# Kernel tuning notes

Hardware: AMD Instinct MI355X
Metric: run time of the kernel (lower is better)

Reference implementation:

```python
import jax, jax.numpy as jnp
import numpy as np

D_MODEL = 1024
N_HEADS = 16
HEAD = D_MODEL // N_HEADS  # 64
B, S = 4, 2048


def setup_inputs() -> dict:
    key = jax.random.key(0)
    ks = jax.random.split(key, 8)
    sd = 1.0 / np.sqrt(D_MODEL)
    return {
        "query": jax.random.normal(ks[0], (B, S, D_MODEL), jnp.float32),
        "key_in": jax.random.normal(ks[1], (B, S, D_MODEL), jnp.float32),
        "value": jax.random.normal(ks[2], (B, S, D_MODEL), jnp.float32),
        # per-head projections stacked: [H, d_model, head_size]
        "Wq": jax.random.normal(ks[3], (N_HEADS, D_MODEL, HEAD), jnp.float32) * sd,
        "Wk": jax.random.normal(ks[4], (N_HEADS, D_MODEL, HEAD), jnp.float32) * sd,
        "Wv": jax.random.normal(ks[5], (N_HEADS, D_MODEL, HEAD), jnp.float32) * sd,
        "Wo": jax.random.normal(ks[6], (D_MODEL, D_MODEL), jnp.float32) * sd,
        "bo": jax.random.normal(ks[7], (D_MODEL,), jnp.float32) * 0.01,
    }


def reference(query, key_in, value, Wq, Wk, Wv, Wo, bo):
    # batched per-head projections: [B,H,S,K]
    q = jnp.einsum("bsd,hdk->bhsk", query, Wq)
    k = jnp.einsum("bsd,hdk->bhsk", key_in, Wk)
    v = jnp.einsum("bsd,hdk->bhsk", value, Wv)
    # NOTE: original scales by sqrt(d_model) (query.shape[-1]), not sqrt(head_size)
    scale = 1.0 / np.sqrt(D_MODEL)
    scores = jnp.einsum("bhsk,bhtk->bhst", q, k) * scale  # [B,H,S,S]
    attn = jax.nn.softmax(scores, axis=-1)
    ctx = jnp.einsum("bhst,bhtk->bhsk", attn, v)  # [B,H,S,K]
    # concat heads -> [B,S,H*K]
    ctx = jnp.transpose(ctx, (0, 2, 1, 3)).reshape(B, S, D_MODEL)
    return ctx @ Wo.T + bo  # output linear (dropout = identity at eval)
```

## Files before the change

kernel.cpp:

```cpp
#include <hip/hip_runtime.h>
#include <stdint.h>

#define DM   1024
#define HD   64
#define SEQ  2048
#define NB   4
#define MR   8192

typedef __bf16  bf16x8 __attribute__((ext_vector_type(8)));
typedef float   f32x4  __attribute__((ext_vector_type(4)));
typedef unsigned short u16x8 __attribute__((ext_vector_type(8)));

__device__ __forceinline__ unsigned short f2bf(float f) {
  union { float f; unsigned u; } x; x.f = f;
  unsigned u = x.u + 0x7fffu + ((x.u >> 16) & 1u);
  return (unsigned short)(u >> 16);
}

__device__ __forceinline__ unsigned pk_bf16(float a, float b) {
  unsigned ua = __builtin_bit_cast(unsigned, a) + 0x8000u;
  unsigned ub = __builtin_bit_cast(unsigned, b) + 0x8000u;
  return __builtin_amdgcn_perm(ub, ua, 0x07060302);
}

__device__ __forceinline__ float fexp2(float x) {
#if __has_builtin(__builtin_amdgcn_exp2f)
  return __builtin_amdgcn_exp2f(x);
#else
  float r; asm("v_exp_f32 %0, %1" : "=v"(r) : "v"(x)); return r;
#endif
}

__device__ __forceinline__ void gld_lds16(const void* g, void* l) {
  __builtin_amdgcn_global_load_lds((const __attribute__((address_space(1))) unsigned int*)g,
                                   (__attribute__((address_space(3))) unsigned int*)l, 16, 0, 0);
}

__global__ __launch_bounds__(256) void cvt3(const float* __restrict__ a, const float* __restrict__ b,
                                            const float* __restrict__ c, unsigned short* __restrict__ oa,
                                            unsigned short* __restrict__ ob, unsigned short* __restrict__ oc) {
  const float* in = (blockIdx.z == 0) ? a : (blockIdx.z == 1) ? b : c;
  unsigned short* out = (blockIdx.z == 0) ? oa : (blockIdx.z == 1) ? ob : oc;
  size_t i = ((size_t)blockIdx.x * 256 + threadIdx.x) * 8;
  float4 x = *(const float4*)(in + i);
  float4 y = *(const float4*)(in + i + 4);
  u16x8 r = { f2bf(x.x), f2bf(x.y), f2bf(x.z), f2bf(x.w), f2bf(y.x), f2bf(y.y), f2bf(y.z), f2bf(y.w) };
  *(u16x8*)(out + i) = r;
}

__global__ __launch_bounds__(256) void wtrans(const float* __restrict__ wq, const float* __restrict__ wk,
                                              const float* __restrict__ wv, unsigned short* __restrict__ wt) {
  __shared__ float tile[64 * 65];
  const float* in = (blockIdx.z == 0) ? wq : (blockIdx.z == 1) ? wk : wv;
  unsigned short* out = wt + ((size_t)blockIdx.z << 20);
  const int h = blockIdx.x >> 4, d0 = (blockIdx.x & 15) * 64;
  const int tid = threadIdx.x;
  const int k = tid & 63, rr = tid >> 6;
#pragma unroll
  for (int j = 0; j < 16; ++j) {
    int row = rr + j * 4;
    tile[row * 65 + k] = in[h * 65536 + (d0 + row) * 64 + k];
  }
  __syncthreads();
  const int dd = tid & 63, kr = tid >> 6;
#pragma unroll
  for (int j = 0; j < 16; ++j) {
    int kk = kr + j * 4;
    out[(size_t)(h * 64 + kk) * 1024 + d0 + dd] = f2bf(tile[dd * 65 + kk]);
  }
}

__global__ __launch_bounds__(256) void cvt1(const float* __restrict__ in, unsigned short* __restrict__ out) {
  size_t i = ((size_t)blockIdx.x * 256 + threadIdx.x) * 8;
  float4 x = *(const float4*)(in + i);
  float4 y = *(const float4*)(in + i + 4);
  u16x8 r = { f2bf(x.x), f2bf(x.y), f2bf(x.z), f2bf(x.w), f2bf(y.x), f2bf(y.y), f2bf(y.z), f2bf(y.w) };
  *(u16x8*)(out + i) = r;
}

template <bool BF16OUT>
__global__ __launch_bounds__(256, 2) void gemm_bt(
    const unsigned short* __restrict__ A0, const unsigned short* __restrict__ A1,
    const unsigned short* __restrict__ A2, const unsigned short* __restrict__ Bt,
    void* __restrict__ Cv, const float* __restrict__ bias) {
  __shared__ char lds[32768];
  char* ldsA = lds;
  char* ldsB = lds + 16384;

  const int tid = threadIdx.x, w = tid >> 6, l = tid & 63;
  const int quad = l >> 4, l15 = l & 15;
  const int z = blockIdx.z;
  const unsigned short* A = (z == 0) ? A0 : (z == 1) ? A1 : A2;
  const unsigned short* B = Bt + (size_t)z * (DM * DM);
  const int lin = blockIdx.y * 8 + blockIdx.x;
  const int swz = (lin & 7) * 64 + (lin >> 3);
  const int bm = (swz >> 3) * 128, bn = (swz & 7) * 128;
  const int wrow = (w >> 1) * 64, wcol = (w & 1) * 64;

  const int srow = w * 32 + (l >> 3);
  const int sc   = ((l & 7) ^ ((l >> 3) & 7)) * 8;
  char* ldsAw = ldsA + (w * 32) * 128;
  char* ldsBw = ldsB + (w * 32) * 128;

  f32x4 acc[4][4];
#pragma unroll
  for (int i = 0; i < 4; ++i)
#pragma unroll
    for (int j = 0; j < 4; ++j) acc[i][j] = (f32x4){0.f, 0.f, 0.f, 0.f};

  for (int kt = 0; kt < DM; kt += 64) {
#pragma unroll
    for (int p = 0; p < 4; ++p) {
      gld_lds16(A + (size_t)(bm + srow + p * 8) * DM + kt + sc, ldsAw + p * 1024);
      gld_lds16(B + (size_t)(bn + srow + p * 8) * DM + kt + sc, ldsBw + p * 1024);
    }
    __syncthreads();
#pragma unroll
    for (int ks = 0; ks < 2; ++ks) {
      bf16x8 af[4], bfr[4];
#pragma unroll
      for (int mt = 0; mt < 4; ++mt) {
        int r = wrow + mt * 16 + l15;
        af[mt] = *(const bf16x8*)(ldsA + r * 128 + (((ks * 4 + quad) ^ (r & 7)) * 16));
      }
#pragma unroll
      for (int nt = 0; nt < 4; ++nt) {
        int r = wcol + nt * 16 + l15;
        bfr[nt] = *(const bf16x8*)(ldsB + r * 128 + (((ks * 4 + quad) ^ (r & 7)) * 16));
      }
#pragma unroll
      for (int mt = 0; mt < 4; ++mt)
#pragma unroll
        for (int nt = 0; nt < 4; ++nt)
          acc[mt][nt] = __builtin_amdgcn_mfma_f32_16x16x32_bf16(af[mt], bfr[nt], acc[mt][nt], 0, 0, 0);
    }
    __syncthreads();
  }

  if constexpr (BF16OUT) {
    unsigned short* C = (unsigned short*)Cv + (size_t)z * ((size_t)MR * DM);
#pragma unroll
    for (int mt = 0; mt < 4; ++mt)
#pragma unroll
      for (int r = 0; r < 4; ++r) {
        size_t row = bm + wrow + mt * 16 + quad * 4 + r;
#pragma unroll
        for (int nt = 0; nt < 4; ++nt)
          C[row * DM + bn + wcol + nt * 16 + l15] = f2bf(acc[mt][nt][r]);
      }
  } else {
    float* C = (float*)Cv;
    float bv[4];
#pragma unroll
    for (int nt = 0; nt < 4; ++nt) bv[nt] = bias[bn + wcol + nt * 16 + l15];
#pragma unroll
    for (int mt = 0; mt < 4; ++mt)
#pragma unroll
      for (int r = 0; r < 4; ++r) {
        size_t row = bm + wrow + mt * 16 + quad * 4 + r;
#pragma unroll
        for (int nt = 0; nt < 4; ++nt)
          C[row * DM + bn + wcol + nt * 16 + l15] = acc[mt][nt][r] + bv[nt];
      }
  }
}

__global__ __launch_bounds__(512, 4) void attn_flash(
    const unsigned short* __restrict__ Qp, const unsigned short* __restrict__ Kp,
    const unsigned short* __restrict__ Vp, unsigned short* __restrict__ Ctx) {
  __shared__ char lds[65536];
  char* ldsK  = lds;
  char* ldsVt = lds + 16384;
  char* ldsP  = lds + 32768;

  const int tid = threadIdx.x, w = tid >> 6, l = tid & 63;
  const int quad = l >> 4, l15 = l & 15;
  const int lin = blockIdx.y * 8 + blockIdx.x;
  const int swz = (lin & 7) * 64 + (lin >> 3);
  const int qt = swz & 7, bh = swz >> 3;
  const int b = bh >> 4, h = bh & 15;
  const size_t rb = (size_t)b * SEQ;
  const int hc = h * HD;

  bf16x8 qf[2][2];
  const int q0 = qt * 256 + w * 32;
#pragma unroll
  for (int mt = 0; mt < 2; ++mt)
#pragma unroll
    for (int ks = 0; ks < 2; ++ks)
      qf[mt][ks] = *(const bf16x8*)(Qp + (rb + q0 + mt * 16 + l15) * DM + hc + ks * 32 + quad * 8);

  f32x4 o[2][4], l_acc[2];
#pragma unroll
  for (int mt = 0; mt < 2; ++mt) {
    l_acc[mt] = (f32x4){0.f, 0.f, 0.f, 0.f};
#pragma unroll
    for (int nt = 0; nt < 4; ++nt) o[mt][nt] = (f32x4){0.f, 0.f, 0.f, 0.f};
  }

  const int sc = ((l & 7) ^ (l >> 3)) * 8;
  const float c2 = 0.045084220027780106f;
  char* prow = ldsP + w * 4096;

  const u16x8 ones_u = {0x3f80, 0x3f80, 0x3f80, 0x3f80, 0x3f80, 0x3f80, 0x3f80, 0x3f80};
  const bf16x8 ones = __builtin_bit_cast(bf16x8, ones_u);

  {
    gld_lds16(Kp + (rb + w * 8 + (l >> 3)) * DM + hc + sc, ldsK + w * 1024);
    u16x8 vr = *(const u16x8*)(Vp + (rb + l) * DM + hc + w * 8);
#pragma unroll
    for (int i = 0; i < 8; ++i) {
      int n = w * 8 + i;
      *(unsigned short*)(ldsVt + n * 128 + (((l >> 3) ^ i) * 16) + (l & 7) * 2) = vr[i];
    }
  }

  for (int kt = 0; kt < SEQ / 64; ++kt) {
    const int kb = kt & 1;
    char* ldsKb = ldsK + kb * 8192;
    char* ldsVb = ldsVt + kb * 8192;
    __syncthreads();

    u16x8 vr;
    const bool pre = (kt < SEQ / 64 - 1);
    if (pre) {
      const size_t krow = rb + (size_t)(kt + 1) * 64;
      gld_lds16(Kp + (krow + w * 8 + (l >> 3)) * DM + hc + sc, ldsK + (kb ^ 1) * 8192 + w * 1024);
      vr = *(const u16x8*)(Vp + (krow + l) * DM + hc + w * 8);
    }

    f32x4 s[2][4];
#pragma unroll
    for (int mt = 0; mt < 2; ++mt)
#pragma unroll
      for (int ct = 0; ct < 4; ++ct) s[mt][ct] = (f32x4){0.f, 0.f, 0.f, 0.f};
    __builtin_amdgcn_s_setprio(1);
#pragma unroll
    for (int ks = 0; ks < 2; ++ks)
#pragma unroll
      for (int ct = 0; ct < 4; ++ct) {
        int rt = ct * 16 + l15;
        bf16x8 kf = *(const bf16x8*)(ldsKb + rt * 128 + (((ks * 4 + quad) ^ (rt & 7)) * 16));
        s[0][ct] = __builtin_amdgcn_mfma_f32_16x16x32_bf16(kf, qf[0][ks], s[0][ct], 0, 0, 0);
        s[1][ct] = __builtin_amdgcn_mfma_f32_16x16x32_bf16(kf, qf[1][ks], s[1][ct], 0, 0, 0);
      }
    __builtin_amdgcn_s_setprio(0);

#pragma unroll
    for (int mt = 0; mt < 2; ++mt) {
      char* pr = prow + (mt * 16 + l15) * 128;
      const int co = quad >> 1, bo = (quad & 1) * 8;
#pragma unroll
      for (int ct = 0; ct < 4; ++ct) {
        float p0 = fexp2(__builtin_fmaf(s[mt][ct][0], c2, -2.0f));
        float p1 = fexp2(__builtin_fmaf(s[mt][ct][1], c2, -2.0f));
        float p2 = fexp2(__builtin_fmaf(s[mt][ct][2], c2, -2.0f));
        float p3 = fexp2(__builtin_fmaf(s[mt][ct][3], c2, -2.0f));
        unsigned lo = pk_bf16(p0, p1), hi = pk_bf16(p2, p3);
        unsigned long long pw = (unsigned long long)lo | ((unsigned long long)hi << 32);
        int c = 2 * ct + co;
        *(unsigned long long*)(pr + ((c ^ (l15 & 7)) * 16) + bo) = pw;
      }
    }

    __builtin_amdgcn_s_setprio(1);
#pragma unroll
    for (int ks = 0; ks < 2; ++ks) {
      bf16x8 pf0 = *(const bf16x8*)(prow + l15 * 128 + (((ks * 4 + quad) ^ (l15 & 7)) * 16));
      bf16x8 pf1 = *(const bf16x8*)(prow + (16 + l15) * 128 + (((ks * 4 + quad) ^ (l15 & 7)) * 16));
      l_acc[0] = __builtin_amdgcn_mfma_f32_16x16x32_bf16(pf0, ones, l_acc[0], 0, 0, 0);
      l_acc[1] = __builtin_amdgcn_mfma_f32_16x16x32_bf16(pf1, ones, l_acc[1], 0, 0, 0);
#pragma unroll
      for (int nt = 0; nt < 4; ++nt) {
        int n = nt * 16 + l15;
        bf16x8 vf = *(const bf16x8*)(ldsVb + n * 128 + (((ks * 4 + quad) ^ (n & 7)) * 16));
        o[0][nt] = __builtin_amdgcn_mfma_f32_16x16x32_bf16(pf0, vf, o[0][nt], 0, 0, 0);
        o[1][nt] = __builtin_amdgcn_mfma_f32_16x16x32_bf16(pf1, vf, o[1][nt], 0, 0, 0);
      }
    }
    __builtin_amdgcn_s_setprio(0);

    if (pre) {
      char* vb = ldsVt + (kb ^ 1) * 8192;
#pragma unroll
      for (int i = 0; i < 8; ++i) {
        int n = w * 8 + i;
        *(unsigned short*)(vb + n * 128 + (((l >> 3) ^ i) * 16) + (l & 7) * 2) = vr[i];
      }
    }
  }

#pragma unroll
  for (int mt = 0; mt < 2; ++mt) {
#pragma unroll
    for (int r = 0; r < 4; ++r) {
      float inv = 1.f / l_acc[mt][r];
      size_t row = rb + q0 + mt * 16 + quad * 4 + r;
#pragma unroll
      for (int nt = 0; nt < 4; ++nt)
        Ctx[row * DM + hc + nt * 16 + l15] = f2bf(o[mt][nt][r] * inv);
    }
  }
}

extern "C" void kernel_launch(void* const* d_in, const int* in_sizes, int n_in,
                              void* d_out, int out_size, void* d_ws, size_t ws_size,
                              hipStream_t stream) {
  const float* query  = (const float*)d_in[0];
  const float* key_in = (const float*)d_in[1];
  const float* value  = (const float*)d_in[2];
  const float* Wq = (const float*)d_in[3];
  const float* Wk = (const float*)d_in[4];
  const float* Wv = (const float*)d_in[5];
  const float* Wo = (const float*)d_in[6];
  const float* bo = (const float*)d_in[7];
  float* out = (float*)d_out;

  unsigned short* ws = (unsigned short*)d_ws;
  const size_t NT = (size_t)MR * DM;
  unsigned short* Xq  = ws;
  unsigned short* Xk  = Xq + NT;
  unsigned short* Xv  = Xk + NT;
  unsigned short* Wt  = Xv + NT;
  unsigned short* Wob = Wt + 3 * 1048576;
  unsigned short* Qb  = Wob + 1048576;
  unsigned short* Kb  = Qb + NT;
  unsigned short* Vb  = Kb + NT;
  unsigned short* Cx  = Vb + NT;

  cvt3<<<dim3(4096, 1, 3), 256, 0, stream>>>(query, key_in, value, Xq, Xk, Xv);
  wtrans<<<dim3(256, 1, 3), 256, 0, stream>>>(Wq, Wk, Wv, Wt);
  cvt1<<<dim3(512, 1, 1), 256, 0, stream>>>(Wo, Wob);
  gemm_bt<true><<<dim3(8, 64, 3), 256, 0, stream>>>(Xq, Xk, Xv, Wt, Qb, nullptr);
  attn_flash<<<dim3(8, 64), 512, 0, stream>>>(Qb, Kb, Vb, Cx);
  gemm_bt<false><<<dim3(8, 64, 1), 256, 0, stream>>>(Cx, Cx, Cx, Wob, out, bo);
}
```

Baseline: 305.8 us.

## Halve attention query tile per block to double grid size

Each attention block now handles 128 query rows instead of 256, with each wave doing one 16-row MFMA tile instead of two. The grid doubles to 1024 blocks, LDS drops to 48KB and launch bounds ask for more resident blocks, to raise occupancy and spread work across CUs. In exchange every K/V tile is loaded and transposed into LDS twice as often per query, which adds global and LDS traffic and halves MFMA reuse of each K/V fragment.

```diff
diff --git a/kernel.cpp b/kernel.cpp
--- a/kernel.cpp
+++ b/kernel.cpp
@@ -165,42 +165,37 @@
   }
 }
 
-__global__ __launch_bounds__(512, 4) void attn_flash(
+__global__ __launch_bounds__(512, 6) void attn_flash(
     const unsigned short* __restrict__ Qp, const unsigned short* __restrict__ Kp,
     const unsigned short* __restrict__ Vp, unsigned short* __restrict__ Ctx) {
-  __shared__ char lds[65536];
+  __shared__ char lds[49152];
   char* ldsK  = lds;
   char* ldsVt = lds + 16384;
   char* ldsP  = lds + 32768;
 
   const int tid = threadIdx.x, w = tid >> 6, l = tid & 63;
   const int quad = l >> 4, l15 = l & 15;
-  const int lin = blockIdx.y * 8 + blockIdx.x;
-  const int swz = (lin & 7) * 64 + (lin >> 3);
-  const int qt = swz & 7, bh = swz >> 3;
+  const int lin = blockIdx.y * 16 + blockIdx.x;
+  const int swz = (lin & 7) * 128 + (lin >> 3);
+  const int qt = swz & 15, bh = swz >> 4;
   const int b = bh >> 4, h = bh & 15;
   const size_t rb = (size_t)b * SEQ;
   const int hc = h * HD;
 
-  bf16x8 qf[2][2];
-  const int q0 = qt * 256 + w * 32;
-#pragma unroll
-  for (int mt = 0; mt < 2; ++mt)
-#pragma unroll
-    for (int ks = 0; ks < 2; ++ks)
-      qf[mt][ks] = *(const bf16x8*)(Qp + (rb + q0 + mt * 16 + l15) * DM + hc + ks * 32 + quad * 8);
-
-  f32x4 o[2][4], l_acc[2];
-#pragma unroll
-  for (int mt = 0; mt < 2; ++mt) {
-    l_acc[mt] = (f32x4){0.f, 0.f, 0.f, 0.f};
-#pragma unroll
-    for (int nt = 0; nt < 4; ++nt) o[mt][nt] = (f32x4){0.f, 0.f, 0.f, 0.f};
-  }
+  bf16x8 qf[2];
+  const int q0 = qt * 128 + w * 16;
+#pragma unroll
+  for (int ks = 0; ks < 2; ++ks)
+    qf[ks] = *(const bf16x8*)(Qp + (rb + q0 + l15) * DM + hc + ks * 32 + quad * 8);
+
+  f32x4 o[4], l_acc;
+  l_acc = (f32x4){0.f, 0.f, 0.f, 0.f};
+#pragma unroll
+  for (int nt = 0; nt < 4; ++nt) o[nt] = (f32x4){0.f, 0.f, 0.f, 0.f};
 
   const int sc = ((l & 7) ^ (l >> 3)) * 8;
   const float c2 = 0.045084220027780106f;
-  char* prow = ldsP + w * 4096;
+  char* prow = ldsP + w * 2048;
 
   const u16x8 ones_u = {0x3f80, 0x3f80, 0x3f80, 0x3f80, 0x3f80, 0x3f80, 0x3f80, 0x3f80};
   const bf16x8 ones = __builtin_bit_cast(bf16x8, ones_u);
@@ -229,11 +224,9 @@
       vr = *(const u16x8*)(Vp + (krow + l) * DM + hc + w * 8);
     }
 
-    f32x4 s[2][4];
-#pragma unroll
-    for (int mt = 0; mt < 2; ++mt)
-#pragma unroll
-      for (int ct = 0; ct < 4; ++ct) s[mt][ct] = (f32x4){0.f, 0.f, 0.f, 0.f};
+    f32x4 s[4];
+#pragma unroll
+    for (int ct = 0; ct < 4; ++ct) s[ct] = (f32x4){0.f, 0.f, 0.f, 0.f};
     __builtin_amdgcn_s_setprio(1);
 #pragma unroll
     for (int ks = 0; ks < 2; ++ks)
@@ -241,21 +234,19 @@
       for (int ct = 0; ct < 4; ++ct) {
         int rt = ct * 16 + l15;
         bf16x8 kf = *(const bf16x8*)(ldsKb + rt * 128 + (((ks * 4 + quad) ^ (rt & 7)) * 16));
-        s[0][ct] = __builtin_amdgcn_mfma_f32_16x16x32_bf16(kf, qf[0][ks], s[0][ct], 0, 0, 0);
-        s[1][ct] = __builtin_amdgcn_mfma_f32_16x16x32_bf16(kf, qf[1][ks], s[1][ct], 0, 0, 0);
+        s[ct] = __builtin_amdgcn_mfma_f32_16x16x32_bf16(kf, qf[ks], s[ct], 0, 0, 0);
       }
     __builtin_amdgcn_s_setprio(0);
 
-#pragma unroll
-    for (int mt = 0; mt < 2; ++mt) {
-      char* pr = prow + (mt * 16 + l15) * 128;
+    {
+      char* pr = prow + l15 * 128;
       const int co = quad >> 1, bo = (quad & 1) * 8;
 #pragma unroll
       for (int ct = 0; ct < 4; ++ct) {
-        float p0 = fexp2(__builtin_fmaf(s[mt][ct][0], c2, -2.0f));
-        float p1 = fexp2(__builtin_fmaf(s[mt][ct][1], c2, -2.0f));
-        float p2 = fexp2(__builtin_fmaf(s[mt][ct][2], c2, -2.0f));
-        float p3 = fexp2(__builtin_fmaf(s[mt][ct][3], c2, -2.0f));
+        float p0 = fexp2(__builtin_fmaf(s[ct][0], c2, -2.0f));
+        float p1 = fexp2(__builtin_fmaf(s[ct][1], c2, -2.0f));
+        float p2 = fexp2(__builtin_fmaf(s[ct][2], c2, -2.0f));
+        float p3 = fexp2(__builtin_fmaf(s[ct][3], c2, -2.0f));
         unsigned lo = pk_bf16(p0, p1), hi = pk_bf16(p2, p3);
         unsigned long long pw = (unsigned long long)lo | ((unsigned long long)hi << 32);
         int c = 2 * ct + co;
@@ -267,15 +258,12 @@
 #pragma unroll
     for (int ks = 0; ks < 2; ++ks) {
       bf16x8 pf0 = *(const bf16x8*)(prow + l15 * 128 + (((ks * 4 + quad) ^ (l15 & 7)) * 16));
-      bf16x8 pf1 = *(const bf16x8*)(prow + (16 + l15) * 128 + (((ks * 4 + quad) ^ (l15 & 7)) * 16));
-      l_acc[0] = __builtin_amdgcn_mfma_f32_16x16x32_bf16(pf0, ones, l_acc[0], 0, 0, 0);
-      l_acc[1] = __builtin_amdgcn_mfma_f32_16x16x32_bf16(pf1, ones, l_acc[1], 0, 0, 0);
+      l_acc = __builtin_amdgcn_mfma_f32_16x16x32_bf16(pf0, ones, l_acc, 0, 0, 0);
 #pragma unroll
       for (int nt = 0; nt < 4; ++nt) {
         int n = nt * 16 + l15;
         bf16x8 vf = *(const bf16x8*)(ldsVb + n * 128 + (((ks * 4 + quad) ^ (n & 7)) * 16));
-        o[0][nt] = __builtin_amdgcn_mfma_f32_16x16x32_bf16(pf0, vf, o[0][nt], 0, 0, 0);
-        o[1][nt] = __builtin_amdgcn_mfma_f32_16x16x32_bf16(pf1, vf, o[1][nt], 0, 0, 0);
+        o[nt] = __builtin_amdgcn_mfma_f32_16x16x32_bf16(pf0, vf, o[nt], 0, 0, 0);
       }
     }
     __builtin_amdgcn_s_setprio(0);
@@ -291,15 +279,12 @@
   }
 
 #pragma unroll
-  for (int mt = 0; mt < 2; ++mt) {
-#pragma unroll
-    for (int r = 0; r < 4; ++r) {
-      float inv = 1.f / l_acc[mt][r];
-      size_t row = rb + q0 + mt * 16 + quad * 4 + r;
-#pragma unroll
-      for (int nt = 0; nt < 4; ++nt)
-        Ctx[row * DM + hc + nt * 16 + l15] = f2bf(o[mt][nt][r] * inv);
-    }
+  for (int r = 0; r < 4; ++r) {
+    float inv = 1.f / l_acc[r];
+    size_t row = rb + q0 + quad * 4 + r;
+#pragma unroll
+    for (int nt = 0; nt < 4; ++nt)
+      Ctx[row * DM + hc + nt * 16 + l15] = f2bf(o[nt][r] * inv);
   }
 }
 
@@ -332,6 +317,6 @@
   wtrans<<<dim3(256, 1, 3), 256, 0, stream>>>(Wq, Wk, Wv, Wt);
   cvt1<<<dim3(512, 1, 1), 256, 0, stream>>>(Wo, Wob);
   gemm_bt<true><<<dim3(8, 64, 3), 256, 0, stream>>>(Xq, Xk, Xv, Wt, Qb, nullptr);
-  attn_flash<<<dim3(8, 64), 512, 0, stream>>>(Qb, Kb, Vb, Cx);
+  attn_flash<<<dim3(16, 64), 512, 0, stream>>>(Qb, Kb, Vb, Cx);
   gemm_bt<false><<<dim3(8, 64, 1), 256, 0, stream>>>(Cx, Cx, Cx, Wob, out, bo);
 }
```

New measurement: 330.2 us. 1.08x slower.

## Double-buffer GEMM LDS tiles and merge preprocessing kernels into one launch

Applied to the files above, without the earlier changes.

The projection GEMM now keeps two LDS stages and issues the global-to-LDS loads for the next k-tile before computing on the current one, so load latency overlaps with MFMA work. The three conversion/transpose kernels are fused into a single launch dispatched by block index, saving launch overhead. LDS use per GEMM block doubles to 64KB, which could limit occupancy, and the fused prep grid launches many idle blocks.

```diff
diff --git a/kernel.cpp b/kernel.cpp
--- a/kernel.cpp
+++ b/kernel.cpp
@@ -36,46 +36,49 @@
                                    (__attribute__((address_space(3))) unsigned int*)l, 16, 0, 0);
 }
 
-__global__ __launch_bounds__(256) void cvt3(const float* __restrict__ a, const float* __restrict__ b,
-                                            const float* __restrict__ c, unsigned short* __restrict__ oa,
-                                            unsigned short* __restrict__ ob, unsigned short* __restrict__ oc) {
-  const float* in = (blockIdx.z == 0) ? a : (blockIdx.z == 1) ? b : c;
-  unsigned short* out = (blockIdx.z == 0) ? oa : (blockIdx.z == 1) ? ob : oc;
-  size_t i = ((size_t)blockIdx.x * 256 + threadIdx.x) * 8;
-  float4 x = *(const float4*)(in + i);
-  float4 y = *(const float4*)(in + i + 4);
-  u16x8 r = { f2bf(x.x), f2bf(x.y), f2bf(x.z), f2bf(x.w), f2bf(y.x), f2bf(y.y), f2bf(y.z), f2bf(y.w) };
-  *(u16x8*)(out + i) = r;
-}
-
-__global__ __launch_bounds__(256) void wtrans(const float* __restrict__ wq, const float* __restrict__ wk,
-                                              const float* __restrict__ wv, unsigned short* __restrict__ wt) {
+__global__ __launch_bounds__(256) void prep(
+    const float* __restrict__ qf32, const float* __restrict__ kf32, const float* __restrict__ vf32,
+    unsigned short* __restrict__ xq, unsigned short* __restrict__ xk, unsigned short* __restrict__ xv,
+    const float* __restrict__ wq, const float* __restrict__ wk, const float* __restrict__ wv,
+    unsigned short* __restrict__ wt, const float* __restrict__ wo, unsigned short* __restrict__ wob) {
   __shared__ float tile[64 * 65];
-  const float* in = (blockIdx.z == 0) ? wq : (blockIdx.z == 1) ? wk : wv;
-  unsigned short* out = wt + ((size_t)blockIdx.z << 20);
-  const int h = blockIdx.x >> 4, d0 = (blockIdx.x & 15) * 64;
-  const int tid = threadIdx.x;
-  const int k = tid & 63, rr = tid >> 6;
-#pragma unroll
-  for (int j = 0; j < 16; ++j) {
-    int row = rr + j * 4;
-    tile[row * 65 + k] = in[h * 65536 + (d0 + row) * 64 + k];
-  }
-  __syncthreads();
-  const int dd = tid & 63, kr = tid >> 6;
-#pragma unroll
-  for (int j = 0; j < 16; ++j) {
-    int kk = kr + j * 4;
-    out[(size_t)(h * 64 + kk) * 1024 + d0 + dd] = f2bf(tile[dd * 65 + kk]);
-  }
-}
-
-__global__ __launch_bounds__(256) void cvt1(const float* __restrict__ in, unsigned short* __restrict__ out) {
-  size_t i = ((size_t)blockIdx.x * 256 + threadIdx.x) * 8;
-  float4 x = *(const float4*)(in + i);
-  float4 y = *(const float4*)(in + i + 4);
-  u16x8 r = { f2bf(x.x), f2bf(x.y), f2bf(x.z), f2bf(x.w), f2bf(y.x), f2bf(y.y), f2bf(y.z), f2bf(y.w) };
-  *(u16x8*)(out + i) = r;
+  const int z = blockIdx.z, tid = threadIdx.x;
+  if (z < 3) {
+    const float* in = (z == 0) ? qf32 : (z == 1) ? kf32 : vf32;
+    unsigned short* out = (z == 0) ? xq : (z == 1) ? xk : xv;
+    size_t i = ((size_t)blockIdx.x * 256 + tid) * 8;
+    float4 x = *(const float4*)(in + i);
+    float4 y = *(const float4*)(in + i + 4);
+    u16x8 r = { f2bf(x.x), f2bf(x.y), f2bf(x.z), f2bf(x.w), f2bf(y.x), f2bf(y.y), f2bf(y.z), f2bf(y.w) };
+    *(u16x8*)(out + i) = r;
+    return;
+  }
+  const int bx = blockIdx.x;
+  if (bx < 768) {
+    const int zz = bx >> 8, bb = bx & 255;
+    const float* in = (zz == 0) ? wq : (zz == 1) ? wk : wv;
+    unsigned short* out = wt + ((size_t)zz << 20);
+    const int h = bb >> 4, d0 = (bb & 15) * 64;
+    const int k = tid & 63, rr = tid >> 6;
+#pragma unroll
+    for (int j = 0; j < 16; ++j) {
+      int row = rr + j * 4;
+      tile[row * 65 + k] = in[h * 65536 + (d0 + row) * 64 + k];
+    }
+    __syncthreads();
+    const int dd = tid & 63, kr = tid >> 6;
+#pragma unroll
+    for (int j = 0; j < 16; ++j) {
+      int k2 = kr + j * 4;
+      out[(size_t)(h * 64 + k2) * 1024 + d0 + dd] = f2bf(tile[dd * 65 + k2]);
+    }
+  } else if (bx < 1280) {
+    size_t i = ((size_t)(bx - 768) * 256 + tid) * 8;
+    float4 x = *(const float4*)(wo + i);
+    float4 y = *(const float4*)(wo + i + 4);
+    u16x8 r = { f2bf(x.x), f2bf(x.y), f2bf(x.z), f2bf(x.w), f2bf(y.x), f2bf(y.y), f2bf(y.z), f2bf(y.w) };
+    *(u16x8*)(wob + i) = r;
+  }
 }
 
 template <bool BF16OUT>
@@ -83,9 +86,7 @@
     const unsigned short* __restrict__ A0, const unsigned short* __restrict__ A1,
     const unsigned short* __restrict__ A2, const unsigned short* __restrict__ Bt,
     void* __restrict__ Cv, const float* __restrict__ bias) {
-  __shared__ char lds[32768];
-  char* ldsA = lds;
-  char* ldsB = lds + 16384;
+  __shared__ char lds[65536];
 
   const int tid = threadIdx.x, w = tid >> 6, l = tid & 63;
   const int quad = l >> 4, l15 = l & 15;
@@ -99,8 +100,6 @@
 
   const int srow = w * 32 + (l >> 3);
   const int sc   = ((l & 7) ^ ((l >> 3) & 7)) * 8;
-  char* ldsAw = ldsA + (w * 32) * 128;
-  char* ldsBw = ldsB + (w * 32) * 128;
 
   f32x4 acc[4][4];
 #pragma unroll
@@ -108,13 +107,23 @@
 #pragma unroll
     for (int j = 0; j < 4; ++j) acc[i][j] = (f32x4){0.f, 0.f, 0.f, 0.f};
 
+#define STAGEG(buf, kt) do {                                                   \
+    char* dA = lds + (buf) * 32768 + (w * 32) * 128;                           \
+    char* dB = dA + 16384;                                                     \
+    _Pragma("unroll")                                                          \
+    for (int p = 0; p < 4; ++p) {                                              \
+      gld_lds16(A + (size_t)(bm + srow + p * 8) * DM + (kt) + sc, dA + p * 1024); \
+      gld_lds16(B + (size_t)(bn + srow + p * 8) * DM + (kt) + sc, dB + p * 1024); \
+    } } while (0)
+
+  STAGEG(0, 0);
+  __syncthreads();
+  int cur = 0;
+
   for (int kt = 0; kt < DM; kt += 64) {
-#pragma unroll
-    for (int p = 0; p < 4; ++p) {
-      gld_lds16(A + (size_t)(bm + srow + p * 8) * DM + kt + sc, ldsAw + p * 1024);
-      gld_lds16(B + (size_t)(bn + srow + p * 8) * DM + kt + sc, ldsBw + p * 1024);
-    }
-    __syncthreads();
+    if (kt + 64 < DM) STAGEG(cur ^ 1, kt + 64);
+    char* ldsA = lds + cur * 32768;
+    char* ldsB = ldsA + 16384;
 #pragma unroll
     for (int ks = 0; ks < 2; ++ks) {
       bf16x8 af[4], bfr[4];
@@ -135,7 +144,9 @@
           acc[mt][nt] = __builtin_amdgcn_mfma_f32_16x16x32_bf16(af[mt], bfr[nt], acc[mt][nt], 0, 0, 0);
     }
     __syncthreads();
-  }
+    cur ^= 1;
+  }
+#undef STAGEG
 
   if constexpr (BF16OUT) {
     unsigned short* C = (unsigned short*)Cv + (size_t)z * ((size_t)MR * DM);
@@ -328,9 +339,8 @@
   unsigned short* Vb  = Kb + NT;
   unsigned short* Cx  = Vb + NT;
 
-  cvt3<<<dim3(4096, 1, 3), 256, 0, stream>>>(query, key_in, value, Xq, Xk, Xv);
-  wtrans<<<dim3(256, 1, 3), 256, 0, stream>>>(Wq, Wk, Wv, Wt);
-  cvt1<<<dim3(512, 1, 1), 256, 0, stream>>>(Wo, Wob);
+  prep<<<dim3(4096, 1, 4), 256, 0, stream>>>(query, key_in, value, Xq, Xk, Xv,
+                                             Wq, Wk, Wv, Wt, Wo, Wob);
   gemm_bt<true><<<dim3(8, 64, 3), 256, 0, stream>>>(Xq, Xk, Xv, Wt, Qb, nullptr);
   attn_flash<<<dim3(8, 64), 512, 0, stream>>>(Qb, Kb, Vb, Cx);
   gemm_bt<false><<<dim3(8, 64, 1), 256, 0, stream>>>(Cx, Cx, Cx, Wob, out, bo);
```

Measured after the change: 303.2 us. About the same (-0.8%).
